# Performance work log

Measured on AMD Instinct MI355X. Metric: run time of the kernel, lower is better.

Reference implementation:

```python
import jax, jax.numpy as jnp
import numpy as np

B, L, D = 4096, 200, 64


def setup_inputs() -> dict:
    key = jax.random.key(0)
    ks = jax.random.split(key, 7)
    target_key = jax.random.normal(ks[0], (B, D), dtype=jnp.float32)
    item_keys = jax.random.normal(ks[1], (B, L, D), dtype=jnp.float32)
    item_values = jax.random.normal(ks[2], (B, L, D), dtype=jnp.float32)
    mask = jax.random.randint(ks[3], (B, L), 0, 2, dtype=jnp.int32)
    # Linear(D, D, bias=False) weights; torch applies y = x @ W.T
    scale = 1.0 / np.sqrt(D)
    W_target = jax.random.uniform(ks[4], (D, D), jnp.float32, -scale, scale)
    W_item = jax.random.uniform(ks[5], (D, D), jnp.float32, -scale, scale)
    W_value = jax.random.uniform(ks[6], (D, D), jnp.float32, -scale, scale)
    return {
        "target_key": target_key,
        "item_keys": item_keys,
        "item_values": item_values,
        "mask": mask,
        "W_target": W_target,
        "W_item": W_item,
        "W_value": W_value,
    }


def reference(target_key, item_keys, item_values, mask, W_target, W_item, W_value):
    scaler = jnp.float32(D) ** 0.5
    q = target_key @ W_target.T                      # [B, D]
    k = jnp.einsum("bld,ed->ble", item_keys, W_item)   # [B, L, D]
    v = jnp.einsum("bld,ed->ble", item_values, W_value) # [B, L, D]
    # single-query scores: broadcast multiply + reduce over D
    scores = jnp.einsum("bd,bld->bl", q, k) / scaler  # [B, L]
    scores = scores + (-1e8) * (1.0 - mask.astype(scores.dtype))
    w = jax.nn.softmax(scores, axis=1)                # softmax over L
    return jnp.einsum("bl,bld->bd", w, v)             # [B, D]
```

## Files before the change

### kernel.cpp

```cpp
#include <hip/hip_runtime.h>


#define B_ 4096
#define L_ 200
#define D_ 64
#define WIN 12

#define PIN() __builtin_amdgcn_sched_barrier(0x387)

__global__ __launch_bounds__(256, 4) void ta_kernel(
    const float* __restrict__ tk,
    const float* __restrict__ ik,
    const float* __restrict__ iv,
    const int*   __restrict__ mask,
    const float* __restrict__ Wt,
    const float* __restrict__ Wi,
    const float* __restrict__ Wv,
    float* __restrict__ out)
{
  const int lane = threadIdx.x & 63;
  const int b    = blockIdx.x * 4 + (threadIdx.x >> 6);
  const int c    = lane & 15;
  const int rg   = lane >> 4;

  const float4* tkb4 = (const float4*)(tk + (size_t)b * D_);
  const float4* Wt4  = (const float4*)Wt;
  float q = 0.f;
#pragma unroll
  for (int j = 0; j < 16; ++j) {
    float4 w = Wt4[lane * 16 + j];
    float4 x = tkb4[j];
    q += w.x * x.x + w.y * x.y + w.z * x.z + w.w * x.w;
  }
  float qt = 0.f;
#pragma unroll
  for (int e = 0; e < 64; ++e) {
    float qe = __shfl(q, e, 64);
    qt += qe * Wi[e * D_ + lane];
  }
  float4 qc;
  qc.x = __shfl(qt, 4 * c + 0, 64);
  qc.y = __shfl(qt, 4 * c + 1, 64);
  qc.z = __shfl(qt, 4 * c + 2, 64);
  qc.w = __shfl(qt, 4 * c + 3, 64);

  float bias[4];
#pragma unroll
  for (int j = 0; j < 4; ++j) {
    int r = 64 * j + 4 * c + rg;
    if (j < 3 || c < 2) {
      int m = mask[(size_t)b * L_ + r];
      bias[j] = m ? 0.f : -1e8f;
    } else {
      bias[j] = 0.f;
    }
  }

  const float4* ik4 = (const float4*)(ik + (size_t)b * (L_ * D_));
  const float4* iv4 = (const float4*)(iv + (size_t)b * (L_ * D_));

  float4 w_[WIN];
#pragma unroll
  for (int i = 0; i < WIN; ++i) w_[i] = ik4[i * 64 + lane];
  PIN();

  float s[4] = {-3e38f, -3e38f, -3e38f, -3e38f};
#pragma unroll
  for (int it = 0; it < 50; ++it) {
    float4 kv = w_[it % WIN];
    if (it + WIN < 50) w_[it % WIN] = ik4[(it + WIN) * 64 + lane];
    float p = kv.x * qc.x + kv.y * qc.y + kv.z * qc.z + kv.w * qc.w;
    p += __shfl_xor(p, 8, 64);
    p += __shfl_xor(p, 4, 64);
    p += __shfl_xor(p, 2, 64);
    p += __shfl_xor(p, 1, 64);
    if (c == (it & 15)) s[it >> 4] = p * 0.125f + bias[it >> 4];
    PIN();
  }

#pragma unroll
  for (int i = 0; i < WIN; ++i) w_[i] = iv4[i * 64 + lane];
  PIN();

  float mx = fmaxf(fmaxf(s[0], s[1]), fmaxf(s[2], s[3]));
#pragma unroll
  for (int off = 32; off >= 1; off >>= 1)
    mx = fmaxf(mx, __shfl_xor(mx, off, 64));
  float e_[4];
#pragma unroll
  for (int j = 0; j < 4; ++j) e_[j] = __expf(s[j] - mx);
  float tt = e_[0] + e_[1] + e_[2] + e_[3];
#pragma unroll
  for (int off = 32; off >= 1; off >>= 1)
    tt += __shfl_xor(tt, off, 64);
  float rtot = 1.0f / tt;

  float4 acc = make_float4(0.f, 0.f, 0.f, 0.f);
#pragma unroll
  for (int it = 0; it < 50; ++it) {
    float4 vv = w_[it % WIN];
    if (it + WIN < 50) w_[it % WIN] = iv4[(it + WIN) * 64 + lane];
    float wgt = __shfl(e_[it >> 4], (lane & 48) | (it & 15), 64);
    acc.x += wgt * vv.x;
    acc.y += wgt * vv.y;
    acc.z += wgt * vv.z;
    acc.w += wgt * vv.w;
    PIN();
  }

  acc.x *= rtot; acc.y *= rtot; acc.z *= rtot; acc.w *= rtot;
  acc.x += __shfl_xor(acc.x, 16, 64); acc.x += __shfl_xor(acc.x, 32, 64);
  acc.y += __shfl_xor(acc.y, 16, 64); acc.y += __shfl_xor(acc.y, 32, 64);
  acc.z += __shfl_xor(acc.z, 16, 64); acc.z += __shfl_xor(acc.z, 32, 64);
  acc.w += __shfl_xor(acc.w, 16, 64); acc.w += __shfl_xor(acc.w, 32, 64);

  const float4* Wv4 = (const float4*)Wv;
  float o = 0.f;
#pragma unroll
  for (int c2 = 0; c2 < 16; ++c2) {
    float sx = __shfl(acc.x, c2, 64);
    float sy = __shfl(acc.y, c2, 64);
    float sz = __shfl(acc.z, c2, 64);
    float sw = __shfl(acc.w, c2, 64);
    float4 w4 = Wv4[lane * 16 + c2];
    o += sx * w4.x + sy * w4.y + sz * w4.z + sw * w4.w;
  }
  out[(size_t)b * D_ + lane] = o;
}

extern "C" void kernel_launch(void* const* d_in, const int* in_sizes, int n_in,
                              void* d_out, int out_size, void* d_ws, size_t ws_size,
                              hipStream_t stream) {
  const float* tk   = (const float*)d_in[0];
  const float* ik   = (const float*)d_in[1];
  const float* iv   = (const float*)d_in[2];
  const int*   mask = (const int*)  d_in[3];
  const float* Wt   = (const float*)d_in[4];
  const float* Wi   = (const float*)d_in[5];
  const float* Wv   = (const float*)d_in[6];
  float* out = (float*)d_out;

  ta_kernel<<<B_ / 4, 256, 0, stream>>>(tk, ik, iv, mask, Wt, Wi, Wv, out);
}
```

Measured before the change: 429.8 us.

## Hand-pipeline K/V loads with inline asm and explicit vmcnt waits

```diff
diff --git a/kernel.cpp b/kernel.cpp
--- a/kernel.cpp
+++ b/kernel.cpp
@@ -6,7 +6,11 @@
 #define D_ 64
 #define WIN 12
 
-#define PIN() __builtin_amdgcn_sched_barrier(0x387)
+#define SB0() __builtin_amdgcn_sched_barrier(0)
+#define GLOAD(dst, ptr) \
+  asm volatile("global_load_dwordx4 %0, %1, off" : "=v"(dst) : "v"(ptr))
+#define VWAITN(n) \
+  do { asm volatile("s_waitcnt vmcnt(" #n ")" ::: "memory"); SB0(); } while (0)
 
 __global__ __launch_bounds__(256, 4) void ta_kernel(
     const float* __restrict__ tk,
@@ -34,10 +38,8 @@
   }
   float qt = 0.f;
 #pragma unroll
-  for (int e = 0; e < 64; ++e) {
-    float qe = __shfl(q, e, 64);
-    qt += qe * Wi[e * D_ + lane];
-  }
+  for (int e = 0; e < 64; ++e)
+    qt += __shfl(q, e, 64) * Wi[e * D_ + lane];
   float4 qc;
   qc.x = __shfl(qt, 4 * c + 0, 64);
   qc.y = __shfl(qt, 4 * c + 1, 64);
@@ -48,39 +50,45 @@
 #pragma unroll
   for (int j = 0; j < 4; ++j) {
     int r = 64 * j + 4 * c + rg;
-    if (j < 3 || c < 2) {
-      int m = mask[(size_t)b * L_ + r];
-      bias[j] = m ? 0.f : -1e8f;
-    } else {
-      bias[j] = 0.f;
-    }
+    bias[j] = 0.f;
+    if (r < L_) bias[j] = mask[(size_t)b * L_ + r] ? 0.f : -1e8f;
   }
 
   const float4* ik4 = (const float4*)(ik + (size_t)b * (L_ * D_));
   const float4* iv4 = (const float4*)(iv + (size_t)b * (L_ * D_));
 
   float4 w_[WIN];
+  float  s[4] = {-3e38f, -3e38f, -3e38f, -3e38f};
+
+  VWAITN(0);
+
 #pragma unroll
-  for (int i = 0; i < WIN; ++i) w_[i] = ik4[i * 64 + lane];
-  PIN();
+  for (int i = 0; i < WIN; ++i) GLOAD(w_[i], ik4 + i * 64 + lane);
 
-  float s[4] = {-3e38f, -3e38f, -3e38f, -3e38f};
 #pragma unroll
-  for (int it = 0; it < 50; ++it) {
+  for (int it = 0; it < 38; ++it) {
+    VWAITN(11);
     float4 kv = w_[it % WIN];
-    if (it + WIN < 50) w_[it % WIN] = ik4[(it + WIN) * 64 + lane];
+    GLOAD(w_[it % WIN], ik4 + (it + 12) * 64 + lane);
     float p = kv.x * qc.x + kv.y * qc.y + kv.z * qc.z + kv.w * qc.w;
     p += __shfl_xor(p, 8, 64);
     p += __shfl_xor(p, 4, 64);
     p += __shfl_xor(p, 2, 64);
     p += __shfl_xor(p, 1, 64);
     if (c == (it & 15)) s[it >> 4] = p * 0.125f + bias[it >> 4];
-    PIN();
   }
-
 #pragma unroll
-  for (int i = 0; i < WIN; ++i) w_[i] = iv4[i * 64 + lane];
-  PIN();
+  for (int it = 38; it < 50; ++it) {
+    VWAITN(11);
+    float4 kv = w_[it % WIN];
+    GLOAD(w_[it % WIN], iv4 + (it - 38) * 64 + lane);
+    float p = kv.x * qc.x + kv.y * qc.y + kv.z * qc.z + kv.w * qc.w;
+    p += __shfl_xor(p, 8, 64);
+    p += __shfl_xor(p, 4, 64);
+    p += __shfl_xor(p, 2, 64);
+    p += __shfl_xor(p, 1, 64);
+    if (c == (it & 15)) s[it >> 4] = p * 0.125f + bias[it >> 4];
+  }
 
   float mx = fmaxf(fmaxf(s[0], s[1]), fmaxf(s[2], s[3]));
 #pragma unroll
@@ -97,16 +105,28 @@
 
   float4 acc = make_float4(0.f, 0.f, 0.f, 0.f);
 #pragma unroll
-  for (int it = 0; it < 50; ++it) {
-    float4 vv = w_[it % WIN];
-    if (it + WIN < 50) w_[it % WIN] = iv4[(it + WIN) * 64 + lane];
+  for (int it = 0; it < 38; ++it) {
+    VWAITN(11);
+    float4 vv = w_[(it + 2) % WIN];
+    GLOAD(w_[(it + 2) % WIN], iv4 + (it + 12) * 64 + lane);
     float wgt = __shfl(e_[it >> 4], (lane & 48) | (it & 15), 64);
     acc.x += wgt * vv.x;
     acc.y += wgt * vv.y;
     acc.z += wgt * vv.z;
     acc.w += wgt * vv.w;
-    PIN();
   }
+#define VTAIL(IT, N)                                                   \
+  do {                                                                 \
+    asm volatile("s_waitcnt vmcnt(" #N ")" ::: "memory"); SB0();       \
+    float4 vv = w_[((IT) + 2) % WIN];                                  \
+    float wgt = __shfl(e_[(IT) >> 4], (lane & 48) | ((IT) & 15), 64);  \
+    acc.x += wgt * vv.x; acc.y += wgt * vv.y;                          \
+    acc.z += wgt * vv.z; acc.w += wgt * vv.w;                          \
+  } while (0)
+  VTAIL(38, 11); VTAIL(39, 10); VTAIL(40, 9); VTAIL(41, 8);
+  VTAIL(42, 7);  VTAIL(43, 6);  VTAIL(44, 5); VTAIL(45, 4);
+  VTAIL(46, 3);  VTAIL(47, 2);  VTAIL(48, 1); VTAIL(49, 0);
+#undef VTAIL
 
   acc.x *= rtot; acc.y *= rtot; acc.z *= rtot; acc.w *= rtot;
   acc.x += __shfl_xor(acc.x, 16, 64); acc.x += __shfl_xor(acc.x, 32, 64);
```

After: 421.8 us. Within noise of the previous version (-1.9%).

## Hand-schedule global loads with inline asm and explicit vmcnt waits

Applied to the files above, without the earlier changes.

```diff
diff --git a/kernel.cpp b/kernel.cpp
--- a/kernel.cpp
+++ b/kernel.cpp
@@ -4,9 +4,12 @@
 #define B_ 4096
 #define L_ 200
 #define D_ 64
-#define WIN 12
 
-#define PIN() __builtin_amdgcn_sched_barrier(0x387)
+#define SB0() __builtin_amdgcn_sched_barrier(0)
+#define GLOAD(dst, ptr) \
+  asm volatile("global_load_dwordx4 %0, %1, off" : "=v"(dst) : "v"(ptr))
+#define VWAITN(n) \
+  do { asm volatile("s_waitcnt vmcnt(" #n ")" ::: "memory"); SB0(); } while (0)
 
 __global__ __launch_bounds__(256, 4) void ta_kernel(
     const float* __restrict__ tk,
@@ -34,79 +37,116 @@
   }
   float qt = 0.f;
 #pragma unroll
-  for (int e = 0; e < 64; ++e) {
-    float qe = __shfl(q, e, 64);
-    qt += qe * Wi[e * D_ + lane];
-  }
+  for (int e = 0; e < 64; ++e)
+    qt += __shfl(q, e, 64) * Wi[e * D_ + lane];
   float4 qc;
   qc.x = __shfl(qt, 4 * c + 0, 64);
   qc.y = __shfl(qt, 4 * c + 1, 64);
   qc.z = __shfl(qt, 4 * c + 2, 64);
   qc.w = __shfl(qt, 4 * c + 3, 64);
 
-  float bias[4];
-#pragma unroll
-  for (int j = 0; j < 4; ++j) {
-    int r = 64 * j + 4 * c + rg;
-    if (j < 3 || c < 2) {
-      int m = mask[(size_t)b * L_ + r];
-      bias[j] = m ? 0.f : -1e8f;
-    } else {
-      bias[j] = 0.f;
-    }
-  }
+  const int* mb = mask + (size_t)b * L_;
+  float bias0 = mb[      4 * c + rg] ? 0.f : -1e8f;
+  float bias1 = mb[ 64 + 4 * c + rg] ? 0.f : -1e8f;
+  float bias2 = mb[128 + 4 * c + rg] ? 0.f : -1e8f;
+  float bias3 = (c < 2) ? (mb[192 + 4 * c + rg] ? 0.f : -1e8f) : 0.f;
 
   const float4* ik4 = (const float4*)(ik + (size_t)b * (L_ * D_));
   const float4* iv4 = (const float4*)(iv + (size_t)b * (L_ * D_));
 
-  float4 w_[WIN];
-#pragma unroll
-  for (int i = 0; i < WIN; ++i) w_[i] = ik4[i * 64 + lane];
-  PIN();
+  float4 w0, w1, w2, w3, w4, w5, w6, w7, w8, w9, w10, w11;
+  float s0 = -3e38f, s1 = -3e38f, s2 = -3e38f, s3 = -3e38f;
 
-  float s[4] = {-3e38f, -3e38f, -3e38f, -3e38f};
-#pragma unroll
-  for (int it = 0; it < 50; ++it) {
-    float4 kv = w_[it % WIN];
-    if (it + WIN < 50) w_[it % WIN] = ik4[(it + WIN) * 64 + lane];
-    float p = kv.x * qc.x + kv.y * qc.y + kv.z * qc.z + kv.w * qc.w;
-    p += __shfl_xor(p, 8, 64);
-    p += __shfl_xor(p, 4, 64);
-    p += __shfl_xor(p, 2, 64);
-    p += __shfl_xor(p, 1, 64);
-    if (c == (it & 15)) s[it >> 4] = p * 0.125f + bias[it >> 4];
-    PIN();
-  }
+  VWAITN(0);
 
-#pragma unroll
-  for (int i = 0; i < WIN; ++i) w_[i] = iv4[i * 64 + lane];
-  PIN();
+  GLOAD(w0,  ik4 +  0 * 64 + lane);  GLOAD(w1,  ik4 +  1 * 64 + lane);
+  GLOAD(w2,  ik4 +  2 * 64 + lane);  GLOAD(w3,  ik4 +  3 * 64 + lane);
+  GLOAD(w4,  ik4 +  4 * 64 + lane);  GLOAD(w5,  ik4 +  5 * 64 + lane);
+  GLOAD(w6,  ik4 +  6 * 64 + lane);  GLOAD(w7,  ik4 +  7 * 64 + lane);
+  GLOAD(w8,  ik4 +  8 * 64 + lane);  GLOAD(w9,  ik4 +  9 * 64 + lane);
+  GLOAD(w10, ik4 + 10 * 64 + lane);  GLOAD(w11, ik4 + 11 * 64 + lane);
 
-  float mx = fmaxf(fmaxf(s[0], s[1]), fmaxf(s[2], s[3]));
+#define KS(IT, SLOT, J)                                                  \
+  do {                                                                   \
+    VWAITN(11);                                                          \
+    float4 kv = w##SLOT;                                                 \
+    GLOAD(w##SLOT, ik4 + ((IT) + 12) * 64 + lane);                       \
+    float p = kv.x * qc.x + kv.y * qc.y + kv.z * qc.z + kv.w * qc.w;     \
+    p += __shfl_xor(p, 8, 64); p += __shfl_xor(p, 4, 64);                \
+    p += __shfl_xor(p, 2, 64); p += __shfl_xor(p, 1, 64);                \
+    if (c == ((IT) & 15)) s##J = p * 0.125f + bias##J;                   \
+  } while (0)
+#define KT(IT, SLOT, J, VOFF)                                            \
+  do {                                                                   \
+    VWAITN(11);                                                          \
+    float4 kv = w##SLOT;                                                 \
+    GLOAD(w##SLOT, iv4 + (VOFF) * 64 + lane);                            \
+    float p = kv.x * qc.x + kv.y * qc.y + kv.z * qc.z + kv.w * qc.w;     \
+    p += __shfl_xor(p, 8, 64); p += __shfl_xor(p, 4, 64);                \
+    p += __shfl_xor(p, 2, 64); p += __shfl_xor(p, 1, 64);                \
+    if (c == ((IT) & 15)) s##J = p * 0.125f + bias##J;                   \
+  } while (0)
+
+  KS(0,0,0);   KS(1,1,0);   KS(2,2,0);   KS(3,3,0);
+  KS(4,4,0);   KS(5,5,0);   KS(6,6,0);   KS(7,7,0);
+  KS(8,8,0);   KS(9,9,0);   KS(10,10,0); KS(11,11,0);
+  KS(12,0,0);  KS(13,1,0);  KS(14,2,0);  KS(15,3,0);
+  KS(16,4,1);  KS(17,5,1);  KS(18,6,1);  KS(19,7,1);
+  KS(20,8,1);  KS(21,9,1);  KS(22,10,1); KS(23,11,1);
+  KS(24,0,1);  KS(25,1,1);  KS(26,2,1);  KS(27,3,1);
+  KS(28,4,1);  KS(29,5,1);  KS(30,6,1);  KS(31,7,1);
+  KS(32,8,2);  KS(33,9,2);  KS(34,10,2); KS(35,11,2);
+  KS(36,0,2);  KS(37,1,2);
+  KT(38,2,2,0);  KT(39,3,2,1);  KT(40,4,2,2);  KT(41,5,2,3);
+  KT(42,6,2,4);  KT(43,7,2,5);  KT(44,8,2,6);  KT(45,9,2,7);
+  KT(46,10,2,8); KT(47,11,2,9); KT(48,0,3,10); KT(49,1,3,11);
+
+  float mx = fmaxf(fmaxf(s0, s1), fmaxf(s2, s3));
 #pragma unroll
   for (int off = 32; off >= 1; off >>= 1)
     mx = fmaxf(mx, __shfl_xor(mx, off, 64));
-  float e_[4];
-#pragma unroll
-  for (int j = 0; j < 4; ++j) e_[j] = __expf(s[j] - mx);
-  float tt = e_[0] + e_[1] + e_[2] + e_[3];
+  float e0 = __expf(s0 - mx);
+  float e1 = __expf(s1 - mx);
+  float e2 = __expf(s2 - mx);
+  float e3 = __expf(s3 - mx);
+  float tt = e0 + e1 + e2 + e3;
 #pragma unroll
   for (int off = 32; off >= 1; off >>= 1)
     tt += __shfl_xor(tt, off, 64);
   float rtot = 1.0f / tt;
 
   float4 acc = make_float4(0.f, 0.f, 0.f, 0.f);
-#pragma unroll
-  for (int it = 0; it < 50; ++it) {
-    float4 vv = w_[it % WIN];
-    if (it + WIN < 50) w_[it % WIN] = iv4[(it + WIN) * 64 + lane];
-    float wgt = __shfl(e_[it >> 4], (lane & 48) | (it & 15), 64);
-    acc.x += wgt * vv.x;
-    acc.y += wgt * vv.y;
-    acc.z += wgt * vv.z;
-    acc.w += wgt * vv.w;
-    PIN();
-  }
+#define VS(IT, SLOT, J)                                                  \
+  do {                                                                   \
+    VWAITN(11);                                                          \
+    float4 vv = w##SLOT;                                                 \
+    GLOAD(w##SLOT, iv4 + ((IT) + 12) * 64 + lane);                       \
+    float wgt = __shfl(e##J, (lane & 48) | ((IT) & 15), 64);             \
+    acc.x += wgt * vv.x; acc.y += wgt * vv.y;                            \
+    acc.z += wgt * vv.z; acc.w += wgt * vv.w;                            \
+  } while (0)
+#define VT(IT, SLOT, J, N)                                               \
+  do {                                                                   \
+    VWAITN(N);                                                           \
+    float4 vv = w##SLOT;                                                 \
+    float wgt = __shfl(e##J, (lane & 48) | ((IT) & 15), 64);             \
+    acc.x += wgt * vv.x; acc.y += wgt * vv.y;                            \
+    acc.z += wgt * vv.z; acc.w += wgt * vv.w;                            \
+  } while (0)
+
+  VS(0,2,0);   VS(1,3,0);   VS(2,4,0);   VS(3,5,0);
+  VS(4,6,0);   VS(5,7,0);   VS(6,8,0);   VS(7,9,0);
+  VS(8,10,0);  VS(9,11,0);  VS(10,0,0);  VS(11,1,0);
+  VS(12,2,0);  VS(13,3,0);  VS(14,4,0);  VS(15,5,0);
+  VS(16,6,1);  VS(17,7,1);  VS(18,8,1);  VS(19,9,1);
+  VS(20,10,1); VS(21,11,1); VS(22,0,1);  VS(23,1,1);
+  VS(24,2,1);  VS(25,3,1);  VS(26,4,1);  VS(27,5,1);
+  VS(28,6,1);  VS(29,7,1);  VS(30,8,1);  VS(31,9,1);
+  VS(32,10,2); VS(33,11,2); VS(34,0,2);  VS(35,1,2);
+  VS(36,2,2);  VS(37,3,2);
+  VT(38,4,2,11); VT(39,5,2,10); VT(40,6,2,9); VT(41,7,2,8);
+  VT(42,8,2,7);  VT(43,9,2,6);  VT(44,10,2,5); VT(45,11,2,4);
+  VT(46,0,2,3);  VT(47,1,2,2);  VT(48,2,3,1);  VT(49,3,3,0);
 
   acc.x *= rtot; acc.y *= rtot; acc.z *= rtot; acc.w *= rtot;
   acc.x += __shfl_xor(acc.x, 16, 64); acc.x += __shfl_xor(acc.x, 32, 64);
```

Measured after the change: 420.8 us. 1.02x faster.
